# Optimization experiments

Measured on AMD Instinct MI355X. Metric: run time of the kernel, lower is better.

Reference implementation:

```python
import jax, jax.numpy as jnp
import numpy as np

N_USERS = 100000   # n
N_ITEMS = 50000    # m
N_EDGES = 1000000  # observed user-item interactions
D = 64             # embedding dim
ALPHA = 1.0        # Rankformer alpha
CLAMP = 1e-6       # args.rankformer_clamp_value (min clamp on omega norm)


def setup_inputs() -> dict:
    key = jax.random.key(0)
    k1, k2, k3 = jax.random.split(key, 3)
    x = jax.random.normal(k1, (N_USERS + N_ITEMS, D), dtype=jnp.float32)
    u = jax.random.randint(k2, (N_EDGES,), 0, N_USERS, dtype=jnp.int64)
    i = jax.random.randint(k3, (N_EDGES,), 0, N_ITEMS, dtype=jnp.int64)
    return {"x": x, "u": u, "i": i}


def reference(x, u, i):
    seg = jax.ops.segment_sum
    n, m = N_USERS, N_ITEMS
    dt = x.dtype

    # degree of each user; duj = number of non-interacted items
    dui = seg(jnp.ones((u.shape[0],), dt), u, num_segments=n)
    duj = m - dui
    dui = jnp.maximum(dui, 1.0)[:, None]  # [n,1]
    duj = jnp.maximum(duj, 1.0)[:, None]  # [n,1]

    # F.normalize(x): row-wise L2 with eps=1e-12
    xn = x / jnp.maximum(jnp.linalg.norm(x, axis=1, keepdims=True), 1e-12)
    xu, xi = xn[:n], xn[n:]   # normalized user / item features
    vu, vi = x[:n], x[n:]     # raw (value) user / item features

    xi_e = xi[i]              # [E,d] gathered item features per edge
    vi_e = vi[i]
    xui = jnp.sum(xu[u] * xi_e, axis=1, keepdims=True)  # [E,1] edge scores

    sxi = seg(xi_e, u, num_segments=n)          # sum of pos-item x per user
    sxj = jnp.sum(xi, axis=0) - sxi             # rest (neg) sum
    svi = seg(vi_e, u, num_segments=n)
    svj = jnp.sum(vi, axis=0) - svi

    b_pos = jnp.sum(xu * sxi, axis=1, keepdims=True) / dui
    b_neg = jnp.sum(xu * sxj, axis=1, keepdims=True) / duj

    du1 = jnp.sum(xu * sxi, axis=1, keepdims=True) / dui - b_neg + ALPHA
    du2 = -jnp.sum(xu * sxj, axis=1, keepdims=True) / duj + b_pos + ALPHA

    di1 = (jnp.sum(xi * seg((xu / dui)[u], i, num_segments=m), axis=1, keepdims=True)
           + seg(((-b_neg + ALPHA) / dui)[u], i, num_segments=m))
    rest_x = jnp.sum(xu / duj, axis=0)[None, :] - seg((xu / duj)[u], i, num_segments=m)
    rest_b = (jnp.sum((b_pos + ALPHA) / duj, axis=0)[None, :]
              - seg(((b_pos + ALPHA) / duj)[u], i, num_segments=m))
    di2 = -jnp.sum(xi * rest_x, axis=1, keepdims=True) + rest_b

    A = seg(xui * vi_e, u, num_segments=n)      # [n,d]
    # xvi.sum(0): S[a,b] = sum_m vi[m,a]*xi[m,b]  (never materialize [m,d,d])
    S = jnp.einsum('ma,mb->ab', vi, xi)
    zu1 = A / dui - svi * (b_neg - ALPHA) / dui
    zu2 = (xu @ S - A) / duj - svj * (b_pos + ALPHA) / duj

    zi1 = (seg(xui * vu[u] / dui[u], i, num_segments=m)
           - seg((vu * (b_neg - ALPHA) / dui)[u], i, num_segments=m))
    # ((xu/duj) outer vu).sum(0): T[a,b] = sum_n (xu/duj)[n,a]*vu[n,b]
    T = jnp.einsum('na,nb->ab', xu / duj, vu)
    rest_v = (jnp.sum(vu * (b_pos + ALPHA) / duj, axis=0)[None, :]
              - seg((vu * (b_pos + ALPHA) / duj)[u], i, num_segments=m))
    zi2 = xi @ T - seg(xui * (vu / duj)[u], i, num_segments=m) - rest_v

    z = jnp.concatenate([zu1 + zu2, zi1 + zi2], axis=0)          # [n+m,d]
    d1 = jnp.maximum(jnp.concatenate([du1, di1], axis=0), CLAMP)  # [n+m,1]
    d2 = jnp.maximum(jnp.concatenate([du2, di2], axis=0), CLAMP)
    return z / (d1 + d2)
```

## Files before the change

### kernel.cpp

```cpp
#include <hip/hip_runtime.h>

#define NU 100000
#define NI 50000
#define DD 64
#define ALPHA_C 1.0f
#define EPS_CLAMP 1e-6f

typedef _Float16 h4 __attribute__((ext_vector_type(4)));

__device__ __forceinline__ float rsum16(float v) {
  v += __shfl_xor(v, 1, 64);
  v += __shfl_xor(v, 2, 64);
  v += __shfl_xor(v, 4, 64);
  v += __shfl_xor(v, 8, 64);
  return v;
}
__device__ __forceinline__ float xgrp2(float v) {
  v += __shfl_xor(v, 16, 64);
  v += __shfl_xor(v, 32, 64);
  return v;
}
__device__ __forceinline__ float wsum(float v) { return xgrp2(rsum16(v)); }

__global__ void k_norm_sums(const float* __restrict__ x, float* __restrict__ inv_norm,
                            float* __restrict__ nrm, h4* __restrict__ xnih,
                            h4* __restrict__ vuh,
                            float* __restrict__ sum_xi, float* __restrict__ sum_vi) {
  __shared__ float sx_s[DD], sv_s[DD];
  if (threadIdx.x < DD) { sx_s[threadIdx.x] = 0.f; sv_s[threadIdx.x] = 0.f; }
  __syncthreads();
  int lane = threadIdx.x & 63;
  int g = lane >> 4, c = lane & 15;
  int wid = blockIdx.x * 4 + (threadIdx.x >> 6);
  int nw  = gridDim.x * 4;
  float sx0=0,sx1=0,sx2=0,sx3=0, sv0=0,sv1=0,sv2=0,sv3=0;
  for (int rb = wid * 4; rb < NU + NI; rb += nw * 4) {
    int r = rb + g;
    const float4 v4 = *(const float4*)(x + (size_t)r * DD + 4 * c);
    float p = v4.x*v4.x + v4.y*v4.y + v4.z*v4.z + v4.w*v4.w;
    p = rsum16(p);
    float nc  = fmaxf(sqrtf(p), 1e-12f);
    float inv = 1.0f / nc;
    if (c == 0) inv_norm[r] = inv;
    if (r >= NU) {
      int j = r - NU;
      if (c == 0) nrm[j] = nc;
      float xn0 = v4.x*inv, xn1 = v4.y*inv, xn2 = v4.z*inv, xn3 = v4.w*inv;
      h4 hw = { (_Float16)xn0, (_Float16)xn1, (_Float16)xn2, (_Float16)xn3 };
      xnih[(size_t)j * 16 + c] = hw;
      sv0 += v4.x; sv1 += v4.y; sv2 += v4.z; sv3 += v4.w;
      sx0 += xn0;  sx1 += xn1;  sx2 += xn2;  sx3 += xn3;
    } else {
      h4 hw = { (_Float16)v4.x, (_Float16)v4.y, (_Float16)v4.z, (_Float16)v4.w };
      vuh[(size_t)r * 16 + c] = hw;
    }
  }
  atomicAdd(&sx_s[4*c+0], sx0); atomicAdd(&sx_s[4*c+1], sx1);
  atomicAdd(&sx_s[4*c+2], sx2); atomicAdd(&sx_s[4*c+3], sx3);
  atomicAdd(&sv_s[4*c+0], sv0); atomicAdd(&sv_s[4*c+1], sv1);
  atomicAdd(&sv_s[4*c+2], sv2); atomicAdd(&sv_s[4*c+3], sv3);
  __syncthreads();
  if (threadIdx.x < DD) {
    atomicAdd(&sum_xi[threadIdx.x], sx_s[threadIdx.x]);
    atomicAdd(&sum_vi[threadIdx.x], sv_s[threadIdx.x]);
  }
}

__global__ void k_count2(const int* __restrict__ u, const int* __restrict__ it,
                         int* __restrict__ du, int* __restrict__ di,
                         int* __restrict__ ru_, int* __restrict__ ri_, int E) {
  int t = blockIdx.x * blockDim.x + threadIdx.x;
  int stride = gridDim.x * blockDim.x;
  for (int e = t; e < E; e += stride) {
    ru_[e] = atomicAdd(&du[u[e]], 1);
    ri_[e] = atomicAdd(&di[it[e]], 1);
  }
}

__global__ void k_scan2(const int* __restrict__ cnt0, int n0, int* __restrict__ off0,
                        const int* __restrict__ cnt1, int n1, int* __restrict__ off1) {
  const int* cnt = blockIdx.x ? cnt1 : cnt0;
  int n          = blockIdx.x ? n1   : n0;
  int* off       = blockIdx.x ? off1 : off0;
  __shared__ int wsum_s[16];
  __shared__ int carry_s;
  int t = threadIdx.x, lane = t & 63, wv = t >> 6;
  if (t == 0) carry_s = 0;
  __syncthreads();
  for (int base = 0; base < n; base += 1024 * 8) {
    int v[8];
    int s = 0;
    int i0 = base + t * 8;
#pragma unroll
    for (int k = 0; k < 8; ++k) {
      int idx = i0 + k;
      v[k] = (idx < n) ? cnt[idx] : 0;
      s += v[k];
    }
    int incl = s;
#pragma unroll
    for (int d = 1; d < 64; d <<= 1) {
      int t2 = __shfl_up(incl, d, 64);
      if (lane >= d) incl += t2;
    }
    if (lane == 63) wsum_s[wv] = incl;
    __syncthreads();
    int woff = 0, total = 0;
#pragma unroll
    for (int w = 0; w < 16; ++w) {
      int ws_v = wsum_s[w];
      woff += (w < wv) ? ws_v : 0;
      total += ws_v;
    }
    int excl = carry_s + woff + incl - s;
#pragma unroll
    for (int k = 0; k < 8; ++k) {
      int idx = i0 + k;
      if (idx < n) off[idx] = excl;
      excl += v[k];
    }
    __syncthreads();
    if (t == 0) carry_s += total;
    __syncthreads();
  }
  if (t == 0) off[n] = carry_s;
}

#define GRID_OUT 256
#define GS_OUT 85
#define OCH 32
__global__ void k_fused_os(const float* __restrict__ x, const float* __restrict__ inv_norm,
                           const int* __restrict__ du, float* __restrict__ part,
                           const int* __restrict__ u, const int* __restrict__ it,
                           const int* __restrict__ ru_, const int* __restrict__ ri_,
                           const int* __restrict__ uoff, const int* __restrict__ ioff, int E,
                           int* __restrict__ uev, unsigned long long* __restrict__ iue) {
  __shared__ float rows_s[OCH * DD];
  __shared__ float w_s[OCH];
  if ((int)blockIdx.x >= GRID_OUT) {
    int bloc = (int)blockIdx.x - GRID_OUT;
    int nb = (int)gridDim.x - GRID_OUT;
    int t = bloc * blockDim.x + threadIdx.x;
    int stride = nb * blockDim.x;
    for (int e = t; e < E; e += stride) {
      int uu = __builtin_nontemporal_load(&u[e]);
      int ii = __builtin_nontemporal_load(&it[e]);
      int pu = uoff[uu] + __builtin_nontemporal_load(&ru_[e]);
      int pi = ioff[ii] + __builtin_nontemporal_load(&ri_[e]);
      __builtin_nontemporal_store(ii, &uev[pu]);
      unsigned long long packed = (unsigned long long)(unsigned)uu |
                                  ((unsigned long long)(unsigned)pu << 32);
      __builtin_nontemporal_store(packed, &iue[pi]);
    }
    return;
  }
  bool isT = (int)blockIdx.x >= GS_OUT;
  int bloc = isT ? (int)blockIdx.x - GS_OUT : (int)blockIdx.x;
  int nb   = isT ? (GRID_OUT - GS_OUT) : GS_OUT;
  int nrows = isT ? NU : NI;
  int row0  = isT ? 0 : NU;
  int t = threadIdx.x;
  int a0 = (t >> 4) << 2;
  int b0 = (t & 15) << 2;
  float acc[4][4];
#pragma unroll
  for (int i = 0; i < 4; ++i)
#pragma unroll
    for (int j = 0; j < 4; ++j) acc[i][j] = 0.f;
  int nch = (nrows + OCH - 1) / OCH;
  int limit = row0 + nrows;
  for (int ch = bloc; ch < nch; ch += nb) {
    int rbase = row0 + ch * OCH;
    __syncthreads();
    {
      const float4* src = (const float4*)(x + (size_t)rbase * DD);
      float4* dst = (float4*)rows_s;
      int r1 = rbase + (t >> 4);
      dst[t] = (r1 < limit) ? src[t] : make_float4(0.f, 0.f, 0.f, 0.f);
      int r2 = rbase + ((t + 256) >> 4);
      dst[t + 256] = (r2 < limit) ? src[t + 256] : make_float4(0.f, 0.f, 0.f, 0.f);
      if (t < OCH) {
        int r = rbase + t;
        float w = 0.f;
        if (r < limit) {
          w = inv_norm[r];
          if (isT) w /= fmaxf((float)NI - (float)du[r], 1.0f);
        }
        w_s[t] = w;
      }
    }
    __syncthreads();
#pragma unroll 8
    for (int r = 0; r < OCH; ++r) {
      float w = w_s[r];
      const float4 av = *(const float4*)(rows_s + r * DD + a0);
      const float4 bv = *(const float4*)(rows_s + r * DD + b0);
      float wa0 = av.x * w, wa1 = av.y * w, wa2 = av.z * w, wa3 = av.w * w;
      acc[0][0] += wa0 * bv.x; acc[0][1] += wa0 * bv.y; acc[0][2] += wa0 * bv.z; acc[0][3] += wa0 * bv.w;
      acc[1][0] += wa1 * bv.x; acc[1][1] += wa1 * bv.y; acc[1][2] += wa1 * bv.z; acc[1][3] += wa1 * bv.w;
      acc[2][0] += wa2 * bv.x; acc[2][1] += wa2 * bv.y; acc[2][2] += wa2 * bv.z; acc[2][3] += wa2 * bv.w;
      acc[3][0] += wa3 * bv.x; acc[3][1] += wa3 * bv.y; acc[3][2] += wa3 * bv.z; acc[3][3] += wa3 * bv.w;
    }
  }
  float* dst = part + (size_t)blockIdx.x * (DD * DD);
#pragma unroll
  for (int i = 0; i < 4; ++i)
    *(float4*)(dst + (size_t)(a0 + i) * DD + b0) =
        make_float4(acc[i][0], acc[i][1], acc[i][2], acc[i][3]);
}

__global__ void k_redST(const float* __restrict__ part,
                        float* __restrict__ Smat, float* __restrict__ Tmat) {
  int k = blockIdx.x * blockDim.x + threadIdx.x;
  if (k < DD * DD) {
    float s = 0.f;
    for (int b = 0; b < GS_OUT; ++b) s += part[(size_t)b * (DD * DD) + k];
    Smat[k] = s;
  } else {
    int kk = k - DD * DD;
    float s = 0.f;
    for (int b = GS_OUT; b < GRID_OUT; ++b) s += part[(size_t)b * (DD * DD) + kk];
    Tmat[kk] = s;
  }
}

__global__ void k_matvec(const float* __restrict__ x, const float* __restrict__ inv_norm,
                         const float* __restrict__ Smat, const float* __restrict__ Tmat,
                         float* __restrict__ out, int gU) {
  bool isI = (int)blockIdx.x >= gU;
  const float* M = isI ? Tmat : Smat;
  int row0  = isI ? NU : 0;
  int nrows = isI ? NI : NU;
  int bloc  = isI ? (int)blockIdx.x - gU : (int)blockIdx.x;
  int nb    = isI ? (int)gridDim.x - gU : gU;
  int lane = threadIdx.x & 63;
  float m_reg[DD];
#pragma unroll
  for (int a = 0; a < DD; ++a) m_reg[a] = M[a * DD + lane];
  int wid = bloc * (blockDim.x >> 6) + (threadIdx.x >> 6);
  int nw  = nb * (blockDim.x >> 6);
  for (int rr = wid; rr < nrows; rr += nw) {
    int r = row0 + rr;
    float v = x[(size_t)r * DD + lane] * inv_norm[r];
    float a0 = 0.f, a1 = 0.f, a2 = 0.f, a3 = 0.f;
#pragma unroll
    for (int a = 0; a < DD; a += 4) {
      a0 += __shfl(v, a)     * m_reg[a];
      a1 += __shfl(v, a + 1) * m_reg[a + 1];
      a2 += __shfl(v, a + 2) * m_reg[a + 2];
      a3 += __shfl(v, a + 3) * m_reg[a + 3];
    }
    out[(size_t)r * DD + lane] = (a0 + a1) + (a2 + a3);
  }
}

__global__ void k_user5(const float* __restrict__ x, const float* __restrict__ inv_norm,
                        const float* __restrict__ nrm, const h4* __restrict__ xnih,
                        const int* __restrict__ uoff, const int* __restrict__ uev,
                        const float* __restrict__ sum_xi, const float* __restrict__ sum_vi,
                        float* __restrict__ d_raw, float4* __restrict__ usc,
                        float* __restrict__ out,
                        float* __restrict__ Gx, float* __restrict__ Gv, float* __restrict__ Gb) {
  __shared__ float gx_s[DD], gv_s[DD], gb_s;
  if (threadIdx.x < DD) { gx_s[threadIdx.x] = 0.f; gv_s[threadIdx.x] = 0.f; }
  if (threadIdx.x == 0) gb_s = 0.f;
  __syncthreads();
  int lane = threadIdx.x & 63;
  int g = lane >> 4, c = lane & 15;
  float gmask = (g == 0) ? 1.f : 0.f;
  int wid = blockIdx.x * (blockDim.x >> 6) + (threadIdx.x >> 6);
  int nw  = gridDim.x * (blockDim.x >> 6);
  const float4 sx4  = *(const float4*)(sum_xi + 4 * c);
  const float4 svl4 = *(const float4*)(sum_vi + 4 * c);
  float gxa0=0,gxa1=0,gxa2=0,gxa3=0, gva0=0,gva1=0,gva2=0,gva3=0, gb=0.f;
  for (int uu = wid; uu < NU; uu += nw) {
    size_t ru = (size_t)uu * DD;
    int beg = uoff[uu], end2 = uoff[uu + 1];
    int deg = end2 - beg;
    float a1 = 1.0f / fmaxf((float)deg, 1.0f);
    float a2 = 1.0f / fmaxf((float)(NI - deg), 1.0f);
    float invu = inv_norm[uu];
    const float4 v4 = *(const float4*)(x + ru + 4 * c);
    float4 xu4 = make_float4(v4.x*invu, v4.y*invu, v4.z*invu, v4.w*invu);
    float Av0=0,Av1=0,Av2=0,Av3=0, sv0=0,sv1=0,sv2=0,sv3=0;
    float sA = 0.f;
    for (int base = beg; base < end2; base += 64) {
      int nb2 = end2 - base; if (nb2 > 64) nb2 = 64;
      int ii_l = 0; float nc_l = 0.f;
      if (lane < nb2) {
        ii_l = uev[base + lane];
        nc_l = nrm[ii_l];
      }
      for (int k0 = 0; k0 < nb2; k0 += 4) {
        int   ii = __shfl(ii_l, k0 + g);
        float nc = __shfl(nc_l, k0 + g);
        float f  = (k0 + g < nb2) ? 1.f : 0.f;
        h4 hv = xnih[(size_t)ii * 16 + c];
        float r0 = (float)hv.x, r1 = (float)hv.y, r2 = (float)hv.z, r3 = (float)hv.w;
        float p = xu4.x*r0 + xu4.y*r1 + xu4.z*r2 + xu4.w*r3;
        float d = f * rsum16(p);
        float w = d * nc;
        Av0 += w * r0; Av1 += w * r1; Av2 += w * r2; Av3 += w * r3;
        sv0 += nc * r0; sv1 += nc * r1; sv2 += nc * r2; sv3 += nc * r3;
        sA += d;
        if (c == 0 && k0 + g < nb2) d_raw[base + k0 + g] = d;
      }
    }
    sA  = xgrp2(sA);
    Av0 = xgrp2(Av0); Av1 = xgrp2(Av1); Av2 = xgrp2(Av2); Av3 = xgrp2(Av3);
    sv0 = xgrp2(sv0); sv1 = xgrp2(sv1); sv2 = xgrp2(sv2); sv3 = xgrp2(sv3);
    float bp = sA * a1;
    float pbn = xu4.x*sx4.x + xu4.y*sx4.y + xu4.z*sx4.z + xu4.w*sx4.w;
    float bn = (rsum16(pbn) - sA) * a2;
    float s1 = (ALPHA_C - bn) * a1;
    float s2 = (bp + ALPHA_C) * a2;
    if (lane == 0) usc[uu] = make_float4(a1, a2, s1, s2);
    const float4 xs4 = *(const float4*)(out + ru + 4 * c);
    float c12 = s1 + s2, a12 = a1 - a2;
    float rden = 1.0f / (2.0f * fmaxf(bp - bn + ALPHA_C, EPS_CLAMP));
    float o0 = (Av0 * a12 + sv0 * c12 + xs4.x * a2 - svl4.x * s2) * rden;
    float o1 = (Av1 * a12 + sv1 * c12 + xs4.y * a2 - svl4.y * s2) * rden;
    float o2 = (Av2 * a12 + sv2 * c12 + xs4.z * a2 - svl4.z * s2) * rden;
    float o3 = (Av3 * a12 + sv3 * c12 + xs4.w * a2 - svl4.w * s2) * rden;
    if (g == 0) *(float4*)(out + ru + 4 * c) = make_float4(o0, o1, o2, o3);
    float t2 = a2 * gmask, t3 = s2 * gmask;
    gxa0 += t2 * xu4.x; gxa1 += t2 * xu4.y; gxa2 += t2 * xu4.z; gxa3 += t2 * xu4.w;
    gva0 += t3 * v4.x;  gva1 += t3 * v4.y;  gva2 += t3 * v4.z;  gva3 += t3 * v4.w;
    if (lane == 0) gb += s2;
  }
  if (g == 0) {
    atomicAdd(&gx_s[4*c+0], gxa0); atomicAdd(&gx_s[4*c+1], gxa1);
    atomicAdd(&gx_s[4*c+2], gxa2); atomicAdd(&gx_s[4*c+3], gxa3);
    atomicAdd(&gv_s[4*c+0], gva0); atomicAdd(&gv_s[4*c+1], gva1);
    atomicAdd(&gv_s[4*c+2], gva2); atomicAdd(&gv_s[4*c+3], gva3);
  }
  if (lane == 0) atomicAdd(&gb_s, gb);
  __syncthreads();
  if (threadIdx.x < DD) {
    atomicAdd(&Gx[threadIdx.x], gx_s[threadIdx.x]);
    atomicAdd(&Gv[threadIdx.x], gv_s[threadIdx.x]);
  }
  if (threadIdx.x == 0) atomicAdd(Gb, gb_s);
}

__global__ void k_item5(const float* __restrict__ x, const float* __restrict__ inv_norm,
                        const h4* __restrict__ vuh,
                        const int* __restrict__ ioff, const uint2* __restrict__ iue,
                        const float* __restrict__ d_raw, const float4* __restrict__ usc,
                        const float* __restrict__ Gx, const float* __restrict__ Gv,
                        const float* __restrict__ Gb, float* __restrict__ out) {
  int lane = threadIdx.x & 63;
  int g = lane >> 4, c = lane & 15;
  int wid = blockIdx.x * (blockDim.x >> 6) + (threadIdx.x >> 6);
  int nw  = gridDim.x * (blockDim.x >> 6);
  const float4 Gx4 = *(const float4*)(Gx + 4 * c);
  const float4 Gv4 = *(const float4*)(Gv + 4 * c);
  float gb = *Gb;
  for (int j = wid; j < NI; j += nw) {
    int r = NU + j;
    size_t rr = (size_t)r * DD;
    float invi = inv_norm[r];
    const float4 vi4 = *(const float4*)(x + rr + 4 * c);
    float4 xi4 = make_float4(vi4.x*invi, vi4.y*invi, vi4.z*invi, vi4.w*invi);
    int beg = ioff[j], end2 = ioff[j + 1];
    float W0=0,W1=0,W2=0,W3=0, q1=0.f, q2=0.f;
    for (int base = beg; base < end2; base += 64) {
      int nb2 = end2 - base; if (nb2 > 64) nb2 = 64;
      int uu_l = 0; float glx = 0.f;
      if (lane < nb2) {
        uint2 m = iue[base + lane];
        uu_l = (int)m.x;
        float d = d_raw[m.y];
        float4 cc = usc[uu_l];
        float t1 = d * cc.x + cc.z;
        float t2 = d * cc.y - cc.w;
        q1 += t1; q2 += t2;
        glx = t1 - t2;
      }
      for (int k0 = 0; k0 < nb2; k0 += 4) {
        int   ua = __shfl(uu_l, k0 + g);
        float ge = __shfl(glx,  k0 + g);
        h4 hv = vuh[(size_t)ua * 16 + c];
        W0 += ge * (float)hv.x; W1 += ge * (float)hv.y;
        W2 += ge * (float)hv.z; W3 += ge * (float)hv.w;
      }
    }
    q1 = wsum(q1); q2 = wsum(q2);
    W0 = xgrp2(W0); W1 = xgrp2(W1); W2 = xgrp2(W2); W3 = xgrp2(W3);
    float pd = xi4.x*Gx4.x + xi4.y*Gx4.y + xi4.z*Gx4.z + xi4.w*Gx4.w;
    float di1 = q1;
    float di2 = -rsum16(pd) + q2 + gb;
    const float4 xt4 = *(const float4*)(out + rr + 4 * c);
    float rden = 1.0f / (fmaxf(di1, EPS_CLAMP) + fmaxf(di2, EPS_CLAMP));
    float o0 = (W0 + xt4.x - Gv4.x) * rden;
    float o1 = (W1 + xt4.y - Gv4.y) * rden;
    float o2 = (W2 + xt4.z - Gv4.z) * rden;
    float o3 = (W3 + xt4.w - Gv4.w) * rden;
    if (g == 0) *(float4*)(out + rr + 4 * c) = make_float4(o0, o1, o2, o3);
  }
}

extern "C" void kernel_launch(void* const* d_in, const int* in_sizes, int n_in,
                              void* d_out, int out_size, void* d_ws, size_t ws_size,
                              hipStream_t stream) {
  const float* x  = (const float*)d_in[0];
  const int*   u  = (const int*)d_in[1];
  const int*   it = (const int*)d_in[2];
  float* out = (float*)d_out;
  const int E = in_sizes[1];

  char* wsb = (char*)d_ws;
  size_t off = 0;
  auto alloc = [&](size_t elems) { void* p = wsb + off; off += elems * 4; return p; };

  int*   du     = (int*)alloc(100016);
  int*   di     = (int*)alloc(50016);
  float* sum_xi = (float*)alloc(64);
  float* sum_vi = (float*)alloc(64);
  float* Gx     = (float*)alloc(64);
  float* Gv     = (float*)alloc(64);
  float* Gb     = (float*)alloc(16);
  size_t zero_bytes = off;

  float* Smat   = (float*)alloc(4096);
  float* Tmat   = (float*)alloc(4096);
  float* part   = (float*)alloc((size_t)GRID_OUT * 4096);
  float*  inv_norm = (float*)alloc(150016);
  float*  nrm      = (float*)alloc(50016);
  h4*     xnih     = (h4*)alloc((size_t)NI * 32);
  h4*     vuh      = (h4*)alloc((size_t)NU * 32);
  int*    uoff     = (int*)alloc(100016);
  int*    ioff     = (int*)alloc(50016);
  int*    ru_      = (int*)alloc(1000000);
  int*    ri_      = (int*)alloc(1000000);
  int*    uev      = (int*)alloc(1000000);
  unsigned long long* iue = (unsigned long long*)alloc(2000000);
  float*  d_raw    = (float*)alloc(1000000);
  float4* usc      = (float4*)alloc(400000);

  hipMemsetAsync(d_ws, 0, zero_bytes, stream);

  k_norm_sums<<<1024, 256, 0, stream>>>(x, inv_norm, nrm, xnih, vuh, sum_xi, sum_vi);
  k_count2<<<2048, 256, 0, stream>>>(u, it, du, di, ru_, ri_, E);
  k_scan2<<<2, 1024, 0, stream>>>(du, NU, uoff, di, NI, ioff);
  k_fused_os<<<GRID_OUT + 4096, 256, 0, stream>>>(x, inv_norm, du, part,
                                                  u, it, ru_, ri_, uoff, ioff, E,
                                                  uev, iue);
  k_redST<<<32, 256, 0, stream>>>(part, Smat, Tmat);
  k_matvec<<<1536, 256, 0, stream>>>(x, inv_norm, Smat, Tmat, out, 1024);
  k_user5<<<2048, 256, 0, stream>>>(x, inv_norm, nrm, xnih, uoff, uev, sum_xi, sum_vi,
                                    d_raw, usc, out, Gx, Gv, Gb);
  k_item5<<<2048, 256, 0, stream>>>(x, inv_norm, vuh, ioff, (const uint2*)iue, d_raw, usc,
                                    Gx, Gv, Gb, out);
}
```

Baseline: 598.7 us.

## Fuse count into norm kernel, shrink rank arrays, unroll gather loops by two

```diff
diff --git a/kernel.cpp b/kernel.cpp
--- a/kernel.cpp
+++ b/kernel.cpp
@@ -22,17 +22,35 @@
 }
 __device__ __forceinline__ float wsum(float v) { return xgrp2(rsum16(v)); }
 
-__global__ void k_norm_sums(const float* __restrict__ x, float* __restrict__ inv_norm,
-                            float* __restrict__ nrm, h4* __restrict__ xnih,
-                            h4* __restrict__ vuh,
-                            float* __restrict__ sum_xi, float* __restrict__ sum_vi) {
+#define GN_NORM 1024
+__global__ void k_norm_count(const float* __restrict__ x, float* __restrict__ inv_norm,
+                             float* __restrict__ nrm, h4* __restrict__ xnih,
+                             h4* __restrict__ vuh,
+                             float* __restrict__ sum_xi, float* __restrict__ sum_vi,
+                             const int* __restrict__ u, const int* __restrict__ it,
+                             int* __restrict__ du, int* __restrict__ di,
+                             unsigned short* __restrict__ ru_, unsigned short* __restrict__ ri_,
+                             int E) {
+  if ((int)blockIdx.x >= GN_NORM) {
+    int bloc = (int)blockIdx.x - GN_NORM;
+    int nb = (int)gridDim.x - GN_NORM;
+    int t = bloc * blockDim.x + threadIdx.x;
+    int stride = nb * blockDim.x;
+    for (int e = t; e < E; e += stride) {
+      int uu = __builtin_nontemporal_load(&u[e]);
+      int ii = __builtin_nontemporal_load(&it[e]);
+      ru_[e] = (unsigned short)atomicAdd(&du[uu], 1);
+      ri_[e] = (unsigned short)atomicAdd(&di[ii], 1);
+    }
+    return;
+  }
   __shared__ float sx_s[DD], sv_s[DD];
   if (threadIdx.x < DD) { sx_s[threadIdx.x] = 0.f; sv_s[threadIdx.x] = 0.f; }
   __syncthreads();
   int lane = threadIdx.x & 63;
   int g = lane >> 4, c = lane & 15;
   int wid = blockIdx.x * 4 + (threadIdx.x >> 6);
-  int nw  = gridDim.x * 4;
+  int nw  = GN_NORM * 4;
   float sx0=0,sx1=0,sx2=0,sx3=0, sv0=0,sv1=0,sv2=0,sv3=0;
   for (int rb = wid * 4; rb < NU + NI; rb += nw * 4) {
     int r = rb + g;
@@ -66,17 +84,6 @@
   }
 }
 
-__global__ void k_count2(const int* __restrict__ u, const int* __restrict__ it,
-                         int* __restrict__ du, int* __restrict__ di,
-                         int* __restrict__ ru_, int* __restrict__ ri_, int E) {
-  int t = blockIdx.x * blockDim.x + threadIdx.x;
-  int stride = gridDim.x * blockDim.x;
-  for (int e = t; e < E; e += stride) {
-    ru_[e] = atomicAdd(&du[u[e]], 1);
-    ri_[e] = atomicAdd(&di[it[e]], 1);
-  }
-}
-
 __global__ void k_scan2(const int* __restrict__ cnt0, int n0, int* __restrict__ off0,
                         const int* __restrict__ cnt1, int n1, int* __restrict__ off1) {
   const int* cnt = blockIdx.x ? cnt1 : cnt0;
@@ -132,7 +139,8 @@
 __global__ void k_fused_os(const float* __restrict__ x, const float* __restrict__ inv_norm,
                            const int* __restrict__ du, float* __restrict__ part,
                            const int* __restrict__ u, const int* __restrict__ it,
-                           const int* __restrict__ ru_, const int* __restrict__ ri_,
+                           const unsigned short* __restrict__ ru_,
+                           const unsigned short* __restrict__ ri_,
                            const int* __restrict__ uoff, const int* __restrict__ ioff, int E,
                            int* __restrict__ uev, unsigned long long* __restrict__ iue) {
   __shared__ float rows_s[OCH * DD];
@@ -145,12 +153,11 @@
     for (int e = t; e < E; e += stride) {
       int uu = __builtin_nontemporal_load(&u[e]);
       int ii = __builtin_nontemporal_load(&it[e]);
-      int pu = uoff[uu] + __builtin_nontemporal_load(&ru_[e]);
-      int pi = ioff[ii] + __builtin_nontemporal_load(&ri_[e]);
-      __builtin_nontemporal_store(ii, &uev[pu]);
-      unsigned long long packed = (unsigned long long)(unsigned)uu |
-                                  ((unsigned long long)(unsigned)pu << 32);
-      __builtin_nontemporal_store(packed, &iue[pi]);
+      int pu = uoff[uu] + (int)__builtin_nontemporal_load(&ru_[e]);
+      int pi = ioff[ii] + (int)__builtin_nontemporal_load(&ri_[e]);
+      uev[pu] = ii;
+      iue[pi] = (unsigned long long)(unsigned)uu |
+                ((unsigned long long)(unsigned)pu << 32);
     }
     return;
   }
@@ -254,7 +261,7 @@
   }
 }
 
-__global__ void k_user5(const float* __restrict__ x, const float* __restrict__ inv_norm,
+__global__ void k_user6(const float* __restrict__ x, const float* __restrict__ inv_norm,
                         const float* __restrict__ nrm, const h4* __restrict__ xnih,
                         const int* __restrict__ uoff, const int* __restrict__ uev,
                         const float* __restrict__ sum_xi, const float* __restrict__ sum_vi,
@@ -291,19 +298,30 @@
         ii_l = uev[base + lane];
         nc_l = nrm[ii_l];
       }
-      for (int k0 = 0; k0 < nb2; k0 += 4) {
-        int   ii = __shfl(ii_l, k0 + g);
-        float nc = __shfl(nc_l, k0 + g);
-        float f  = (k0 + g < nb2) ? 1.f : 0.f;
-        h4 hv = xnih[(size_t)ii * 16 + c];
-        float r0 = (float)hv.x, r1 = (float)hv.y, r2 = (float)hv.z, r3 = (float)hv.w;
-        float p = xu4.x*r0 + xu4.y*r1 + xu4.z*r2 + xu4.w*r3;
-        float d = f * rsum16(p);
-        float w = d * nc;
-        Av0 += w * r0; Av1 += w * r1; Av2 += w * r2; Av3 += w * r3;
-        sv0 += nc * r0; sv1 += nc * r1; sv2 += nc * r2; sv3 += nc * r3;
-        sA += d;
-        if (c == 0 && k0 + g < nb2) d_raw[base + k0 + g] = d;
+      for (int k0 = 0; k0 < nb2; k0 += 8) {
+        int ea = k0 + g, eb = k0 + 4 + g;
+        int   iia = __shfl(ii_l, ea), iib = __shfl(ii_l, eb);
+        float nca = __shfl(nc_l, ea), ncb = __shfl(nc_l, eb);
+        float fa = (ea < nb2) ? 1.f : 0.f;
+        float fb = (eb < nb2) ? 1.f : 0.f;
+        h4 hva = xnih[(size_t)iia * 16 + c];
+        h4 hvb = xnih[(size_t)iib * 16 + c];
+        float a0r = (float)hva.x, a1r = (float)hva.y, a2r = (float)hva.z, a3r = (float)hva.w;
+        float b0r = (float)hvb.x, b1r = (float)hvb.y, b2r = (float)hvb.z, b3r = (float)hvb.w;
+        float pa = xu4.x*a0r + xu4.y*a1r + xu4.z*a2r + xu4.w*a3r;
+        float pb = xu4.x*b0r + xu4.y*b1r + xu4.z*b2r + xu4.w*b3r;
+        float da = fa * rsum16(pa);
+        float db = fb * rsum16(pb);
+        float wa = da * nca, wb = db * ncb;
+        Av0 += wa*a0r + wb*b0r; Av1 += wa*a1r + wb*b1r;
+        Av2 += wa*a2r + wb*b2r; Av3 += wa*a3r + wb*b3r;
+        sv0 += nca*a0r + ncb*b0r; sv1 += nca*a1r + ncb*b1r;
+        sv2 += nca*a2r + ncb*b2r; sv3 += nca*a3r + ncb*b3r;
+        sA += da + db;
+        if (c == 0) {
+          if (ea < nb2) d_raw[base + ea] = da;
+          if (eb < nb2) d_raw[base + eb] = db;
+        }
       }
     }
     sA  = xgrp2(sA);
@@ -343,7 +361,7 @@
   if (threadIdx.x == 0) atomicAdd(Gb, gb_s);
 }
 
-__global__ void k_item5(const float* __restrict__ x, const float* __restrict__ inv_norm,
+__global__ void k_item6(const float* __restrict__ x, const float* __restrict__ inv_norm,
                         const h4* __restrict__ vuh,
                         const int* __restrict__ ioff, const uint2* __restrict__ iue,
                         const float* __restrict__ d_raw, const float4* __restrict__ usc,
@@ -377,12 +395,16 @@
         q1 += t1; q2 += t2;
         glx = t1 - t2;
       }
-      for (int k0 = 0; k0 < nb2; k0 += 4) {
-        int   ua = __shfl(uu_l, k0 + g);
-        float ge = __shfl(glx,  k0 + g);
-        h4 hv = vuh[(size_t)ua * 16 + c];
-        W0 += ge * (float)hv.x; W1 += ge * (float)hv.y;
-        W2 += ge * (float)hv.z; W3 += ge * (float)hv.w;
+      for (int k0 = 0; k0 < nb2; k0 += 8) {
+        int ea = k0 + g, eb = k0 + 4 + g;
+        int   ua = __shfl(uu_l, ea), ub = __shfl(uu_l, eb);
+        float ga = __shfl(glx, ea),  gbn = __shfl(glx, eb);
+        h4 hva = vuh[(size_t)ua * 16 + c];
+        h4 hvb = vuh[(size_t)ub * 16 + c];
+        W0 += ga * (float)hva.x + gbn * (float)hvb.x;
+        W1 += ga * (float)hva.y + gbn * (float)hvb.y;
+        W2 += ga * (float)hva.z + gbn * (float)hvb.z;
+        W3 += ga * (float)hva.w + gbn * (float)hvb.w;
       }
     }
     q1 = wsum(q1); q2 = wsum(q2);
@@ -431,8 +453,8 @@
   h4*     vuh      = (h4*)alloc((size_t)NU * 32);
   int*    uoff     = (int*)alloc(100016);
   int*    ioff     = (int*)alloc(50016);
-  int*    ru_      = (int*)alloc(1000000);
-  int*    ri_      = (int*)alloc(1000000);
+  unsigned short* ru_ = (unsigned short*)alloc(500000);
+  unsigned short* ri_ = (unsigned short*)alloc(500000);
   int*    uev      = (int*)alloc(1000000);
   unsigned long long* iue = (unsigned long long*)alloc(2000000);
   float*  d_raw    = (float*)alloc(1000000);
@@ -440,16 +462,17 @@
 
   hipMemsetAsync(d_ws, 0, zero_bytes, stream);
 
-  k_norm_sums<<<1024, 256, 0, stream>>>(x, inv_norm, nrm, xnih, vuh, sum_xi, sum_vi);
-  k_count2<<<2048, 256, 0, stream>>>(u, it, du, di, ru_, ri_, E);
+  k_norm_count<<<GN_NORM + 1024, 256, 0, stream>>>(x, inv_norm, nrm, xnih, vuh,
+                                                   sum_xi, sum_vi,
+                                                   u, it, du, di, ru_, ri_, E);
   k_scan2<<<2, 1024, 0, stream>>>(du, NU, uoff, di, NI, ioff);
   k_fused_os<<<GRID_OUT + 4096, 256, 0, stream>>>(x, inv_norm, du, part,
                                                   u, it, ru_, ri_, uoff, ioff, E,
                                                   uev, iue);
   k_redST<<<32, 256, 0, stream>>>(part, Smat, Tmat);
   k_matvec<<<1536, 256, 0, stream>>>(x, inv_norm, Smat, Tmat, out, 1024);
-  k_user5<<<2048, 256, 0, stream>>>(x, inv_norm, nrm, xnih, uoff, uev, sum_xi, sum_vi,
+  k_user6<<<4096, 256, 0, stream>>>(x, inv_norm, nrm, xnih, uoff, uev, sum_xi, sum_vi,
                                     d_raw, usc, out, Gx, Gv, Gb);
-  k_item5<<<2048, 256, 0, stream>>>(x, inv_norm, vuh, ioff, (const uint2*)iue, d_raw, usc,
+  k_item6<<<4096, 256, 0, stream>>>(x, inv_norm, vuh, ioff, (const uint2*)iue, d_raw, usc,
                                     Gx, Gv, Gb, out);
 }
```

Measured after the change: 652.7 us. +9.0%, slower.
